# Kernel tuning notes

Measured on AMD Instinct MI355X. Metric: run time of the kernel, lower is better.

The kernel has to match this reference:

```python
import jax, jax.numpy as jnp
import numpy as np

C = 16          # cardinality (hard-coded in GraphHead)
E = 1024        # node_encoding_size == representation_size (residual requires equality)
S = 1024        # spatial_head output size (hard-coded Linear(256,1024))
R = 1024        # representation_size
D = R // C      # sub_repr_size = 64
NS, NO = 64, 256
NUM_ITER = 2
EPS = 1e-5


def _w(key, shape, fan_in):
    return jax.random.normal(key, shape, dtype=jnp.float32) * np.float32((2.0 / fan_in) ** 0.5)


def setup_inputs() -> dict:
    key = jax.random.key(0)
    ks = jax.random.split(key, 16)
    inp = {
        'h': jax.random.normal(ks[0], (NS, E), dtype=jnp.float32),
        'o': jax.random.normal(ks[1], (NO, E), dtype=jnp.float32),
        'spatial': jax.random.normal(ks[2], (NS, NO, S), dtype=jnp.float32),
        # attention_head: MultiBranchFusion(2E, 1024, R, 16)
        'att_w1': _w(ks[3], (C, 2 * E, D), 2 * E), 'att_b1': jnp.zeros((C, D), jnp.float32),
        'att_w2': _w(ks[4], (C, S, D), S),         'att_b2': jnp.zeros((C, D), jnp.float32),
        'att_w3': _w(ks[5], (C, D, R), D),         'att_b3': jnp.zeros((C, R), jnp.float32),
        # sub_to_obj: MessageMBF(E, 1024, R, 'subject', 16)
        's2o_w1': _w(ks[6], (C, E, D), E),         's2o_b1': jnp.zeros((C, D), jnp.float32),
        's2o_w2': _w(ks[7], (C, S, D), S),         's2o_b2': jnp.zeros((C, D), jnp.float32),
        's2o_w3': _w(ks[8], (C, D, R), D),         's2o_b3': jnp.zeros((C, R), jnp.float32),
        # obj_to_sub: MessageMBF(E, 1024, R, 'object', 16)
        'o2s_w1': _w(ks[9], (C, E, D), E),         'o2s_b1': jnp.zeros((C, D), jnp.float32),
        'o2s_w2': _w(ks[10], (C, S, D), S),        'o2s_b2': jnp.zeros((C, D), jnp.float32),
        'o2s_w3': _w(ks[11], (C, D, R), D),        'o2s_b3': jnp.zeros((C, R), jnp.float32),
        # adjacency: Linear(R, 1)
        'adj_w': _w(ks[12], (R, 1), R), 'adj_b': jnp.zeros((1,), jnp.float32),
        # LayerNorms
        'ns_g': jnp.ones((E,), jnp.float32), 'ns_b': jnp.zeros((E,), jnp.float32),
        'no_g': jnp.ones((E,), jnp.float32), 'no_b': jnp.zeros((E,), jnp.float32),
    }
    return inp


def _layernorm(x, g, b):
    m = jnp.mean(x, axis=-1, keepdims=True)
    v = jnp.mean((x - m) ** 2, axis=-1, keepdims=True)
    return (x - m) * jax.lax.rsqrt(v + EPS) * g + b


def _mbf_pair(app, spa, w1, b1, w2, b2, w3, b3):
    # app [ns,no,A], spa [ns,no,S] -> [ns,no,R]; sum over C branches of fc3(relu(fc1*fc2))
    a = jnp.einsum('ija,cad->cijd', app, w1) + b1[:, None, None, :]
    s = jnp.einsum('ijs,csd->cijd', spa, w2) + b2[:, None, None, :]
    g = jax.nn.relu(a * s)
    return jnp.einsum('cijd,cdr->ijr', g, w3) + b3.sum(0)


def _msg_subject(h, spa, w1, b1, w2, b2, w3, b3):
    # MessageMBF subject: broadcast fc1(h) [ns,d] against fc2(spa) [ns,no,d]
    a = jnp.einsum('ia,cad->cid', h, w1) + b1[:, None, :]
    s = jnp.einsum('ijs,csd->cijd', spa, w2) + b2[:, None, None, :]
    g = jax.nn.relu(a[:, :, None, :] * s)
    return jnp.einsum('cijd,cdr->ijr', g, w3) + b3.sum(0)  # [ns,no,R]


def _msg_object(o, spa, w1, b1, w2, b2, w3, b3):
    # MessageMBF object: broadcast fc1(o) [no,d] against fc2(spa) [ns,no,d]
    a = jnp.einsum('ja,cad->cjd', o, w1) + b1[:, None, :]
    s = jnp.einsum('ijs,csd->cijd', spa, w2) + b2[:, None, None, :]
    g = jax.nn.relu(a[:, None, :, :] * s)
    return jnp.einsum('cijd,cdr->ijr', g, w3) + b3.sum(0)  # [ns,no,R]


def reference(h, o, spatial,
              att_w1, att_b1, att_w2, att_b2, att_w3, att_b3,
              s2o_w1, s2o_b1, s2o_w2, s2o_b2, s2o_w3, s2o_b3,
              o2s_w1, o2s_b1, o2s_w2, o2s_b2, o2s_w3, o2s_b3,
              adj_w, adj_b, ns_g, ns_b, no_g, no_b):
    ns, no = h.shape[0], o.shape[0]
    for _ in range(NUM_ITER):
        # edge weights via attention MBF on concatenated pair encodings
        pair_app = jnp.concatenate([
            jnp.broadcast_to(h[:, None, :], (ns, no, E)),
            jnp.broadcast_to(o[None, :, :], (ns, no, E)),
        ], axis=-1)
        w = jax.nn.relu(_mbf_pair(pair_app, spatial, att_w1, att_b1, att_w2, att_b2, att_w3, att_b3))
        adj = jnp.einsum('ijr,rk->ij', w, adj_w) + adj_b[0]  # [ns,no]
        # update subject nodes from object messages
        m_o2s = _msg_object(o, spatial, o2s_w1, o2s_b1, o2s_w2, o2s_b2, o2s_w3, o2s_b3)
        msg_h = jax.nn.relu(jnp.einsum('ij,ijr->ir', jax.nn.softmax(adj, axis=1), m_o2s))
        h = _layernorm(h + msg_h, ns_g, ns_b)
        # update object nodes from (updated) subject messages
        m_s2o = _msg_subject(h, spatial, s2o_w1, s2o_b1, s2o_w2, s2o_b2, s2o_w3, s2o_b3)
        msg_o = jax.nn.relu(jnp.einsum('ij,ijr->jr', jax.nn.softmax(adj, axis=0), m_s2o))
        o = _layernorm(o + msg_o, no_g, no_b)
    return jnp.concatenate([h, o], axis=0)  # [ns+no, E]
```

## Files before the change

### kernel.cpp

```cpp
#include <hip/hip_runtime.h>
#include <cstdint>
#include <cstddef>

typedef _Float16 hf;
typedef _Float16 h8v __attribute__((ext_vector_type(8)));
typedef float f4v __attribute__((ext_vector_type(4)));

#define NS 64
#define NO 256
#define MP 16384
#define KD 1024

__device__ __forceinline__ h8v cvt8(float4 a, float4 b) {
    h8v r;
    r[0] = (hf)a.x; r[1] = (hf)a.y; r[2] = (hf)a.z; r[3] = (hf)a.w;
    r[4] = (hf)b.x; r[5] = (hf)b.y; r[6] = (hf)b.z; r[7] = (hf)b.w;
    return r;
}
__device__ __forceinline__ float f4at(const float4& a, const float4& b, int e) {
    const float* p = e < 4 ? (const float*)&a : (const float*)&b;
    return p[e & 3];
}
__device__ __forceinline__ void gl16(const hf* g, hf* l) {
    __builtin_amdgcn_global_load_lds(
        (const __attribute__((address_space(1))) void*)g,
        (__attribute__((address_space(3))) void*)l, 16, 0, 0);
}

__global__ void k_pack16(const float* __restrict__ src, hf* __restrict__ dst, int n8) {
    int g = blockIdx.x * 256 + threadIdx.x;
    if (g >= n8) return;
    const float4* s4 = (const float4*)src;
    float4 a = s4[2 * g], b = s4[2 * g + 1];
    *(h8v*)(dst + (size_t)g * 8) = cvt8(a, b);
}

struct RoR { const float* src; hf* dhi; hf* dlo; int Asrc; int aOff; };
struct RoRs { RoR r[7]; };
__global__ void k_reorder16b(RoRs RR) {
    const RoR rt = RR.r[blockIdx.z];
    __shared__ float tile[64][65];
    int c = blockIdx.x, a0 = blockIdx.y * 64;
    int t = threadIdx.x, lx = t & 63, ly = t >> 6;
#pragma unroll
    for (int p = 0; p < 16; ++p) {
        int ar = ly + p * 4;
        tile[ar][lx] = rt.src[(size_t)(c * rt.Asrc + rt.aOff + a0 + ar) * 64 + lx];
    }
    __syncthreads();
#pragma unroll
    for (int p = 0; p < 16; ++p) {
        int d = ly + p * 4;
        float v = tile[lx][d];
        hf h = (hf)v;
        size_t idx = (size_t)(c * 64 + d) * 1024 + a0 + lx;
        rt.dhi[idx] = h;
        if (rt.dlo) rt.dlo[idx] = (hf)(v - (float)h);
    }
}

struct TrR { const float* src; hf* dhi; hf* dlo; };
struct TrRs { TrR r[3]; };
__global__ void k_transpose16b(TrRs RR) {
    const TrR rt = RR.r[blockIdx.z];
    __shared__ float tile[64][65];
    int r0 = blockIdx.x * 64, s0 = blockIdx.y * 64;
    int t = threadIdx.x, lx = t & 63, ly = t >> 6;
#pragma unroll
    for (int p = 0; p < 16; ++p) {
        int srow = ly + p * 4;
        tile[srow][lx] = rt.src[(size_t)(s0 + srow) * 1024 + r0 + lx];
    }
    __syncthreads();
#pragma unroll
    for (int p = 0; p < 16; ++p) {
        int rr = ly + p * 4;
        float v = tile[lx][rr];
        hf h = (hf)v;
        size_t idx = (size_t)(r0 + rr) * 1024 + s0 + lx;
        rt.dhi[idx] = h;
        if (rt.dlo) rt.dlo[idx] = (hf)(v - (float)h);
    }
}

__global__ void k_prep_bc(const float* __restrict__ ab2, const float* __restrict__ ob2,
                          const float* __restrict__ sb2, const float* __restrict__ ab3,
                          const float* __restrict__ ob3, const float* __restrict__ sb3,
                          float* __restrict__ b2cat, float* __restrict__ b3a,
                          float* __restrict__ b3o, float* __restrict__ b3s) {
    int g = blockIdx.x * 256 + threadIdx.x;
    if (g >= 1024) return;
    b2cat[g] = ab2[g]; b2cat[1024 + g] = ob2[g]; b2cat[2048 + g] = sb2[g];
    float sa = 0.f, so = 0.f, ss = 0.f;
    for (int c = 0; c < 16; ++c) {
        sa += ab3[c * 1024 + g];
        so += ob3[c * 1024 + g];
        ss += sb3[c * 1024 + g];
    }
    b3a[g] = sa; b3o[g] = so; b3s[g] = ss;
}

__global__ void k_init_ho(const float* __restrict__ h, const float* __restrict__ o,
                          float* __restrict__ outbuf, hf* __restrict__ h16, hf* __restrict__ o16) {
    int g = blockIdx.x * 256 + threadIdx.x;
    if (g < NS * KD) { float v = h[g]; outbuf[g] = v; h16[g] = (hf)v; }
    int g2 = g - NS * KD;
    if (g2 >= 0 && g2 < NO * KD) { float v = o[g2]; outbuf[NS * KD + g2] = v; o16[g2] = (hf)v; }
}

__global__ __launch_bounds__(256, 4) void k_prep_gemm(
    const hf* __restrict__ sp16,
    const hf* __restrict__ Wah, const hf* __restrict__ Wal,
    const hf* __restrict__ Wo2, const hf* __restrict__ Ws2,
    const float* __restrict__ b2cat,
    hf* __restrict__ Sh, hf* __restrict__ Sl,
    hf* __restrict__ So, hf* __restrict__ Ss) {
    __shared__ hf Ah[4096];
    __shared__ hf Bh[4096];
    __shared__ hf Bl[4096];
    const int tid = threadIdx.x;
    int lin = blockIdx.y * 24 + blockIdx.x;
    int xcd = lin & 7, slot = lin >> 3;
    int xn = slot % 24;
    const int m0 = ((xcd << 4) + slot / 24) * 128;
    const int plane = xn >> 3;
    const int nbase = (xn & 7) * 128;
    const hf* Bb = plane == 0 ? Wah : (plane == 1 ? Wo2 : Ws2);
    const bool hasL = (plane == 0);
    const int lane = tid & 63, wid = tid >> 6;
    const int wm = wid >> 1, wn = wid & 1;
    const int lr = lane & 15, lg = lane >> 4;
    const int rsl = (lg ^ ((lr >> 1) & 3)) * 8;

    const int crow = lane >> 2;
    const int gseg = ((lane & 3) ^ ((lane >> 3) & 3)) * 8;
    hf* ldsA0 = Ah + wid * 512;         hf* ldsA1 = Ah + 2048 + wid * 512;
    hf* ldsB0 = Bh + wid * 512;         hf* ldsB1 = Bh + 2048 + wid * 512;
    hf* ldsL0 = Bl + wid * 512;         hf* ldsL1 = Bl + 2048 + wid * 512;
    const hf* gA0 = sp16 + (size_t)(m0 +      wid * 16 + crow) * KD + gseg;
    const hf* gA1 = sp16 + (size_t)(m0 + 64 + wid * 16 + crow) * KD + gseg;
    const hf* gB0 = Bb  + (size_t)(nbase +      wid * 16 + crow) * KD + gseg;
    const hf* gB1 = Bb  + (size_t)(nbase + 64 + wid * 16 + crow) * KD + gseg;
    const hf* gL0 = Wal + (size_t)(nbase +      wid * 16 + crow) * KD + gseg;
    const hf* gL1 = Wal + (size_t)(nbase + 64 + wid * 16 + crow) * KD + gseg;

    f4v acc[4][4];
    f4v zz; zz[0] = 0.f; zz[1] = 0.f; zz[2] = 0.f; zz[3] = 0.f;
#pragma unroll
    for (int a = 0; a < 4; ++a)
#pragma unroll
        for (int b = 0; b < 4; ++b) acc[a][b] = zz;

    for (int t = 0; t < 32; ++t) {
        const int kk = t * 32;
        __syncthreads();
        gl16(gA0 + kk, ldsA0); gl16(gA1 + kk, ldsA1);
        gl16(gB0 + kk, ldsB0); gl16(gB1 + kk, ldsB1);
        if (hasL) { gl16(gL0 + kk, ldsL0); gl16(gL1 + kk, ldsL1); }
        __syncthreads();
        h8v fa[4], fb[4];
#pragma unroll
        for (int x = 0; x < 4; ++x) {
            fa[x] = *(const h8v*)(Ah + (wm * 64 + x * 16 + lr) * 32 + rsl);
            fb[x] = *(const h8v*)(Bh + (wn * 64 + x * 16 + lr) * 32 + rsl);
        }
#pragma unroll
        for (int mi = 0; mi < 4; ++mi)
#pragma unroll
            for (int ni = 0; ni < 4; ++ni)
                acc[mi][ni] = __builtin_amdgcn_mfma_f32_16x16x32_f16(fa[mi], fb[ni], acc[mi][ni], 0, 0, 0);
        if (hasL) {
#pragma unroll
            for (int x = 0; x < 4; ++x)
                fb[x] = *(const h8v*)(Bl + (wn * 64 + x * 16 + lr) * 32 + rsl);
#pragma unroll
            for (int mi = 0; mi < 4; ++mi)
#pragma unroll
                for (int ni = 0; ni < 4; ++ni)
                    acc[mi][ni] = __builtin_amdgcn_mfma_f32_16x16x32_f16(fa[mi], fb[ni], acc[mi][ni], 0, 0, 0);
        }
    }
#pragma unroll
    for (int mi = 0; mi < 4; ++mi)
#pragma unroll
        for (int ni = 0; ni < 4; ++ni)
#pragma unroll
            for (int r = 0; r < 4; ++r) {
                int gr = m0 + wm * 64 + mi * 16 + lg * 4 + r;
                int col = nbase + wn * 64 + ni * 16 + lr;
                float v = acc[mi][ni][r] + b2cat[plane * 1024 + col];
                size_t idx = (size_t)gr * KD + col;
                if (plane == 0) {
                    hf hi = (hf)v;
                    Sh[idx] = hi; Sl[idx] = (hf)(v - (float)hi);
                } else if (plane == 1) So[idx] = (hf)v;
                else Ss[idx] = (hf)v;
            }
}

__global__ __launch_bounds__(256, 3) void k_adj_gemm(
    const hf* __restrict__ Sh, const hf* __restrict__ Sl,
    const float* __restrict__ e1, const float* __restrict__ e2,
    const hf* __restrict__ W3h, const hf* __restrict__ W3l,
    const float* __restrict__ b3, const float* __restrict__ aw,
    float* __restrict__ adjv) {
    __shared__ hf Ah[4096];
    __shared__ hf Bh[4096];
    __shared__ hf Bl[4096];
    const int tid = threadIdx.x;
    int lin = blockIdx.y * 8 + blockIdx.x;
    int xcd = lin & 7, slot = lin >> 3;
    const int nbase = (slot & 7) * 128;
    const int m0 = ((xcd << 4) + (slot >> 3)) * 128;
    const int lane = tid & 63, wid = tid >> 6;
    const int wm = wid >> 1, wn = wid & 1;
    const int lr = lane & 15, lg = lane >> 4;
    const int srow = tid >> 2, sseg = tid & 3;
    const int wo_ = srow * 32 + (sseg ^ ((srow >> 1) & 3)) * 8;
    const int rsl = (lg ^ ((lr >> 1) & 3)) * 8;
    const int ar0 = m0 + srow, ar1 = ar0 + 64;
    const int i0 = ar0 >> 8, j0 = ar0 & 255;
    const int i1 = ar1 >> 8, j1 = ar1 & 255;
    const int ko = sseg * 8;

    f4v acc[4][4];
    f4v zz; zz[0] = 0.f; zz[1] = 0.f; zz[2] = 0.f; zz[3] = 0.f;
#pragma unroll
    for (int a = 0; a < 4; ++a)
#pragma unroll
        for (int b = 0; b < 4; ++b) acc[a][b] = zz;

    h8v sh0, sl0, sh1, sl1;
    float4 ex00, ex01, ey00, ey01, ex10, ex11, ey10, ey11;
    h8v vb0, vb1, wb0, wb1;
    h8v gh0, gh1;
    auto LOAD = [&](int kk) {
        sh0 = *(const h8v*)(Sh + (size_t)ar0 * KD + ko + kk);
        sl0 = *(const h8v*)(Sl + (size_t)ar0 * KD + ko + kk);
        sh1 = *(const h8v*)(Sh + (size_t)ar1 * KD + ko + kk);
        sl1 = *(const h8v*)(Sl + (size_t)ar1 * KD + ko + kk);
        ex00 = *(const float4*)(e1 + (size_t)i0 * KD + ko + kk);
        ex01 = *(const float4*)(e1 + (size_t)i0 * KD + ko + kk + 4);
        ey00 = *(const float4*)(e2 + (size_t)j0 * KD + ko + kk);
        ey01 = *(const float4*)(e2 + (size_t)j0 * KD + ko + kk + 4);
        ex10 = *(const float4*)(e1 + (size_t)i1 * KD + ko + kk);
        ex11 = *(const float4*)(e1 + (size_t)i1 * KD + ko + kk + 4);
        ey10 = *(const float4*)(e2 + (size_t)j1 * KD + ko + kk);
        ey11 = *(const float4*)(e2 + (size_t)j1 * KD + ko + kk + 4);
        vb0 = *(const h8v*)(W3h + (size_t)(nbase + srow) * KD + ko + kk);
        vb1 = *(const h8v*)(W3h + (size_t)(nbase + 64 + srow) * KD + ko + kk);
        wb0 = *(const h8v*)(W3l + (size_t)(nbase + srow) * KD + ko + kk);
        wb1 = *(const h8v*)(W3l + (size_t)(nbase + 64 + srow) * KD + ko + kk);
    };
    auto BUILD = [&]() {
#pragma unroll
        for (int e = 0; e < 8; ++e) {
            float s = (float)sh0[e] + (float)sl0[e];
            float ee = f4at(ex00, ex01, e) + f4at(ey00, ey01, e);
            float gg = ee * s; gg = gg > 0.f ? gg : 0.f;
            gh0[e] = (hf)gg;
        }
#pragma unroll
        for (int e = 0; e < 8; ++e) {
            float s = (float)sh1[e] + (float)sl1[e];
            float ee = f4at(ex10, ex11, e) + f4at(ey10, ey11, e);
            float gg = ee * s; gg = gg > 0.f ? gg : 0.f;
            gh1[e] = (hf)gg;
        }
    };
    LOAD(0);
    BUILD();
    for (int t = 0; t < 32; ++t) {
        __syncthreads();
        *(h8v*)(Ah + wo_) = gh0; *(h8v*)(Ah + 2048 + wo_) = gh1;
        *(h8v*)(Bh + wo_) = vb0; *(h8v*)(Bh + 2048 + wo_) = vb1;
        *(h8v*)(Bl + wo_) = wb0; *(h8v*)(Bl + 2048 + wo_) = wb1;
        __syncthreads();
        if (t + 1 < 32) { LOAD((t + 1) * 32); BUILD(); }
        h8v fa[4], fb[4];
#pragma unroll
        for (int x = 0; x < 4; ++x) {
            fa[x] = *(const h8v*)(Ah + (wm * 64 + x * 16 + lr) * 32 + rsl);
            fb[x] = *(const h8v*)(Bh + (wn * 64 + x * 16 + lr) * 32 + rsl);
        }
#pragma unroll
        for (int mi = 0; mi < 4; ++mi)
#pragma unroll
            for (int ni = 0; ni < 4; ++ni)
                acc[mi][ni] = __builtin_amdgcn_mfma_f32_16x16x32_f16(fa[mi], fb[ni], acc[mi][ni], 0, 0, 0);
#pragma unroll
        for (int x = 0; x < 4; ++x)
            fb[x] = *(const h8v*)(Bl + (wn * 64 + x * 16 + lr) * 32 + rsl);
#pragma unroll
        for (int mi = 0; mi < 4; ++mi)
#pragma unroll
            for (int ni = 0; ni < 4; ++ni)
                acc[mi][ni] = __builtin_amdgcn_mfma_f32_16x16x32_f16(fa[mi], fb[ni], acc[mi][ni], 0, 0, 0);
    }
    float b3v[4], awv[4];
#pragma unroll
    for (int ni = 0; ni < 4; ++ni) {
        int gc = nbase + wn * 64 + ni * 16 + lr;
        b3v[ni] = b3[gc]; awv[ni] = aw[gc];
    }
#pragma unroll
    for (int mi = 0; mi < 4; ++mi)
#pragma unroll
        for (int r = 0; r < 4; ++r) {
            float part = 0.f;
#pragma unroll
            for (int ni = 0; ni < 4; ++ni) {
                float w = acc[mi][ni][r] + b3v[ni];
                w = w > 0.f ? w : 0.f;
                part += w * awv[ni];
            }
            part += __shfl_xor(part, 1);
            part += __shfl_xor(part, 2);
            part += __shfl_xor(part, 4);
            part += __shfl_xor(part, 8);
            if (lr == 0) atomicAdd(adjv + m0 + wm * 64 + mi * 16 + lg * 4 + r, part);
        }
}

struct SRoute { const hf* A; const hf* Bh; const hf* Bl; float* C; const float* bias; int m0; int M; };
struct SRoutes { SRoute r[5]; };

__global__ __launch_bounds__(256) void k_small(SRoutes RR) {
    const SRoute rt = RR.r[blockIdx.y];
    __shared__ hf Ah[4096];
    __shared__ hf Bh[4096];
    __shared__ hf Bl[4096];
    const int tid = threadIdx.x;
    const int n0 = blockIdx.x * 128;
    const int kbeg = blockIdx.z * 128;
    const int lane = tid & 63, wid = tid >> 6;
    const int wm = wid >> 1, wn = wid & 1;
    const int lr = lane & 15, lg = lane >> 4;
    const int srow = tid >> 2, sseg = tid & 3;
    const int wo_ = srow * 32 + (sseg ^ ((srow >> 1) & 3)) * 8;
    const int rsl = (lg ^ ((lr >> 1) & 3)) * 8;
    int ar0 = rt.m0 + srow;      if (ar0 >= rt.M) ar0 = rt.M - 1;
    int ar1 = rt.m0 + 64 + srow; if (ar1 >= rt.M) ar1 = rt.M - 1;
    const bool hasL = rt.Bl != nullptr;
    const int ko = kbeg + sseg * 8;

    f4v acc[4][4];
    f4v zz; zz[0] = 0.f; zz[1] = 0.f; zz[2] = 0.f; zz[3] = 0.f;
#pragma unroll
    for (int a = 0; a < 4; ++a)
#pragma unroll
        for (int b = 0; b < 4; ++b) acc[a][b] = zz;

    h8v va0, va1, vb0, vb1, wb0, wb1;
    auto LOAD = [&](int kk) {
        va0 = *(const h8v*)(rt.A + (size_t)ar0 * KD + ko + kk);
        va1 = *(const h8v*)(rt.A + (size_t)ar1 * KD + ko + kk);
        vb0 = *(const h8v*)(rt.Bh + (size_t)(n0 + srow) * KD + ko + kk);
        vb1 = *(const h8v*)(rt.Bh + (size_t)(n0 + 64 + srow) * KD + ko + kk);
        if (hasL) {
            wb0 = *(const h8v*)(rt.Bl + (size_t)(n0 + srow) * KD + ko + kk);
            wb1 = *(const h8v*)(rt.Bl + (size_t)(n0 + 64 + srow) * KD + ko + kk);
        }
    };
    LOAD(0);
    for (int t = 0; t < 4; ++t) {
        __syncthreads();
        *(h8v*)(Ah + wo_) = va0; *(h8v*)(Ah + 2048 + wo_) = va1;
        *(h8v*)(Bh + wo_) = vb0; *(h8v*)(Bh + 2048 + wo_) = vb1;
        if (hasL) { *(h8v*)(Bl + wo_) = wb0; *(h8v*)(Bl + 2048 + wo_) = wb1; }
        __syncthreads();
        if (t + 1 < 4) LOAD((t + 1) * 32);
        h8v fa[4], fb[4];
#pragma unroll
        for (int x = 0; x < 4; ++x) {
            fa[x] = *(const h8v*)(Ah + (wm * 64 + x * 16 + lr) * 32 + rsl);
            fb[x] = *(const h8v*)(Bh + (wn * 64 + x * 16 + lr) * 32 + rsl);
        }
#pragma unroll
        for (int mi = 0; mi < 4; ++mi)
#pragma unroll
            for (int ni = 0; ni < 4; ++ni)
                acc[mi][ni] = __builtin_amdgcn_mfma_f32_16x16x32_f16(fa[mi], fb[ni], acc[mi][ni], 0, 0, 0);
        if (hasL) {
#pragma unroll
            for (int x = 0; x < 4; ++x)
                fb[x] = *(const h8v*)(Bl + (wn * 64 + x * 16 + lr) * 32 + rsl);
#pragma unroll
            for (int mi = 0; mi < 4; ++mi)
#pragma unroll
                for (int ni = 0; ni < 4; ++ni)
                    acc[mi][ni] = __builtin_amdgcn_mfma_f32_16x16x32_f16(fa[mi], fb[ni], acc[mi][ni], 0, 0, 0);
        }
    }
#pragma unroll
    for (int mi = 0; mi < 4; ++mi)
#pragma unroll
        for (int ni = 0; ni < 4; ++ni)
#pragma unroll
            for (int r = 0; r < 4; ++r) {
                int gr = rt.m0 + wm * 64 + mi * 16 + lg * 4 + r;
                int gc = n0 + wn * 64 + ni * 16 + lr;
                if (gr < rt.M) {
                    float v = acc[mi][ni][r];
                    if (rt.bias && blockIdx.z == 0) v += rt.bias[gc];
                    atomicAdd(rt.C + (size_t)gr * KD + gc, v);
                }
            }
}

__global__ void k_softmax_both(const float* __restrict__ adj, float* __restrict__ p,
                               float* __restrict__ q) {
    int b = blockIdx.x;
    if (b < NS) {
        __shared__ float red[256];
        int i = b, j = threadIdx.x;
        float x = adj[i * 256 + j];
        red[j] = x; __syncthreads();
        for (int s = 128; s > 0; s >>= 1) { if (j < s) red[j] = fmaxf(red[j], red[j + s]); __syncthreads(); }
        float mx = red[0]; __syncthreads();
        float e = __expf(x - mx);
        red[j] = e; __syncthreads();
        for (int s = 128; s > 0; s >>= 1) { if (j < s) red[j] += red[j + s]; __syncthreads(); }
        p[i * 256 + j] = e / red[0];
    } else {
        int j = (b - NS) * 4 + (threadIdx.x >> 6);
        int i = threadIdx.x & 63;
        float x = adj[i * 256 + j];
        float mx = x;
#pragma unroll
        for (int off = 32; off > 0; off >>= 1) mx = fmaxf(mx, __shfl_xor(mx, off));
        float e = __expf(x - mx);
        float s = e;
#pragma unroll
        for (int off = 32; off > 0; off >>= 1) s += __shfl_xor(s, off);
        q[i * 256 + j] = e / s;
    }
}

__global__ void k_build_Gh(const hf* __restrict__ S, const float* __restrict__ aF,
                           const float* __restrict__ p, hf* __restrict__ Gh) {
    __shared__ float pl[256];
    int i = blockIdx.x;
    int k = blockIdx.y * 256 + threadIdx.x;
    pl[threadIdx.x] = p[i * 256 + threadIdx.x];
    __syncthreads();
    const hf* sp = S + (size_t)(i * 256) * KD + k;
    float acc = 0.f;
#pragma unroll 4
    for (int j = 0; j < 256; ++j) {
        float a = aF[(size_t)j * KD + k];
        float s = (float)sp[(size_t)j * KD];
        float g = a * s; g = g > 0.f ? g : 0.f;
        acc += pl[j] * g;
    }
    Gh[(size_t)i * KD + k] = (hf)acc;
}

__global__ void k_build_Go(const hf* __restrict__ S, const float* __restrict__ aF,
                           const float* __restrict__ q, hf* __restrict__ Go) {
    __shared__ float ql[64];
    int j = blockIdx.x;
    int k = blockIdx.y * 256 + threadIdx.x;
    if (threadIdx.x < 64) ql[threadIdx.x] = q[threadIdx.x * 256 + j];
    __syncthreads();
    const hf* sp = S + (size_t)j * KD + k;
    float acc = 0.f;
#pragma unroll 4
    for (int i = 0; i < 64; ++i) {
        float a = aF[(size_t)i * KD + k];
        float s = (float)sp[(size_t)(i * 256) * KD];
        float g = a * s; g = g > 0.f ? g : 0.f;
        acc += ql[i] * g;
    }
    Go[(size_t)j * KD + k] = (hf)acc;
}

__global__ void k_ln_update(float* __restrict__ x, const float* __restrict__ msg,
                            const float* __restrict__ b3, const float* __restrict__ gamma,
                            const float* __restrict__ beta, hf* __restrict__ x16) {
    __shared__ float red[256];
    int r = blockIdx.x, t = threadIdx.x;
    float v[4];
    float s = 0.f;
#pragma unroll
    for (int e = 0; e < 4; ++e) {
        int idx = t + e * 256;
        float mm = msg[(size_t)r * KD + idx] + b3[idx];
        mm = mm > 0.f ? mm : 0.f;
        v[e] = x[(size_t)r * KD + idx] + mm;
        s += v[e];
    }
    red[t] = s; __syncthreads();
    for (int st = 128; st > 0; st >>= 1) { if (t < st) red[t] += red[t + st]; __syncthreads(); }
    float mean = red[0] * (1.f / 1024.f);
    __syncthreads();
    float s2 = 0.f;
#pragma unroll
    for (int e = 0; e < 4; ++e) { float d = v[e] - mean; s2 += d * d; }
    red[t] = s2; __syncthreads();
    for (int st = 128; st > 0; st >>= 1) { if (t < st) red[t] += red[t + st]; __syncthreads(); }
    float var = red[0] * (1.f / 1024.f);
    float rstd = rsqrtf(var + 1e-5f);
#pragma unroll
    for (int e = 0; e < 4; ++e) {
        int idx = t + e * 256;
        float y = (v[e] - mean) * rstd * gamma[idx] + beta[idx];
        x[(size_t)r * KD + idx] = y;
        x16[(size_t)r * KD + idx] = (hf)y;
    }
}

extern "C" void kernel_launch(void* const* d_in, const int* in_sizes, int n_in,
                              void* d_out, int out_size, void* d_ws, size_t ws_size,
                              hipStream_t stream) {
    const float* h_in    = (const float*)d_in[0];
    const float* o_in    = (const float*)d_in[1];
    const float* spatial = (const float*)d_in[2];
    const float* att_w1  = (const float*)d_in[3];
    const float* att_b1  = (const float*)d_in[4];
    const float* att_w2  = (const float*)d_in[5];
    const float* att_b2  = (const float*)d_in[6];
    const float* att_w3  = (const float*)d_in[7];
    const float* att_b3  = (const float*)d_in[8];
    const float* s2o_w1  = (const float*)d_in[9];
    const float* s2o_b1  = (const float*)d_in[10];
    const float* s2o_w2  = (const float*)d_in[11];
    const float* s2o_b2  = (const float*)d_in[12];
    const float* s2o_w3  = (const float*)d_in[13];
    const float* s2o_b3  = (const float*)d_in[14];
    const float* o2s_w1  = (const float*)d_in[15];
    const float* o2s_b1  = (const float*)d_in[16];
    const float* o2s_w2  = (const float*)d_in[17];
    const float* o2s_b2  = (const float*)d_in[18];
    const float* o2s_w3  = (const float*)d_in[19];
    const float* o2s_b3  = (const float*)d_in[20];
    const float* adj_w   = (const float*)d_in[21];
    const float* ns_g    = (const float*)d_in[23];
    const float* ns_b    = (const float*)d_in[24];
    const float* no_g    = (const float*)d_in[25];
    const float* no_b    = (const float*)d_in[26];

    char* ws = (char*)d_ws;
    size_t off = 0;
    auto alloc = [&](size_t bytes) -> char* {
        char* pp = ws + off;
        off += (bytes + 255) & ~(size_t)255;
        return pp;
    };
    const size_t PLANE = (size_t)MP * KD * sizeof(hf);
    const size_t WMAT  = (size_t)1024 * 1024 * sizeof(hf);
    hf* S_att_h = (hf*)alloc(PLANE);
    hf* S_att_l = (hf*)alloc(PLANE);
    hf* S_o2s   = (hf*)alloc(PLANE);
    hf* S_s2o   = (hf*)alloc(PLANE);
    hf* sp16    = (hf*)alloc(PLANE);
    hf* W2att_h = (hf*)alloc(WMAT); hf* W2att_l = (hf*)alloc(WMAT);
    hf* W2o2s   = (hf*)alloc(WMAT);
    hf* W2s2o   = (hf*)alloc(WMAT);
    hf* W1ah_h  = (hf*)alloc(WMAT); hf* W1ah_l  = (hf*)alloc(WMAT);
    hf* W1ao_h  = (hf*)alloc(WMAT); hf* W1ao_l  = (hf*)alloc(WMAT);
    hf* W1o2s   = (hf*)alloc(WMAT);
    hf* W1s2o   = (hf*)alloc(WMAT);
    hf* W3a_h   = (hf*)alloc(WMAT); hf* W3a_l   = (hf*)alloc(WMAT);
    hf* W3o     = (hf*)alloc(WMAT);
    hf* W3s     = (hf*)alloc(WMAT);
    float* b2cat = (float*)alloc(3072 * 4);
    float* b3a   = (float*)alloc(1024 * 4);
    float* b3o   = (float*)alloc(1024 * 4);
    float* b3s   = (float*)alloc(1024 * 4);
    float* fc1h = (float*)alloc((size_t)NS * KD * 4);
    float* fc1o = (float*)alloc((size_t)NO * KD * 4);
    float* aO2S = (float*)alloc((size_t)NO * KD * 4);
    float* aS2O = (float*)alloc((size_t)NS * KD * 4);
    float* msgh = (float*)alloc((size_t)NS * KD * 4);
    float* msgo = (float*)alloc((size_t)NO * KD * 4);
    float* adjv = (float*)alloc((size_t)MP * 4);
    char* zend_ = (char*)(adjv + MP);
    size_t zlen = (size_t)(zend_ - (char*)fc1h);
    float* pbuf = (float*)alloc((size_t)MP * 4);
    float* qbuf = (float*)alloc((size_t)MP * 4);
    hf* h16 = (hf*)alloc((size_t)NS * KD * sizeof(hf));
    hf* o16 = (hf*)alloc((size_t)NO * KD * sizeof(hf));
    hf* Gh  = (hf*)alloc((size_t)NS * KD * sizeof(hf));
    hf* Go  = (hf*)alloc((size_t)NO * KD * sizeof(hf));

    float* hbuf = (float*)d_out;
    float* obuf = (float*)d_out + NS * KD;

    k_pack16<<<dim3(MP * KD / 8 / 256), 256, 0, stream>>>(spatial, sp16, MP * KD / 8);
    {
        RoRs R;
        R.r[0] = { att_w2, W2att_h, W2att_l, 1024, 0 };
        R.r[1] = { o2s_w2, W2o2s, nullptr, 1024, 0 };
        R.r[2] = { s2o_w2, W2s2o, nullptr, 1024, 0 };
        R.r[3] = { att_w1, W1ah_h, W1ah_l, 2048, 0 };
        R.r[4] = { att_w1, W1ao_h, W1ao_l, 2048, 1024 };
        R.r[5] = { o2s_w1, W1o2s, nullptr, 1024, 0 };
        R.r[6] = { s2o_w1, W1s2o, nullptr, 1024, 0 };
        k_reorder16b<<<dim3(16, 16, 7), 256, 0, stream>>>(R);
    }
    {
        TrRs T;
        T.r[0] = { att_w3, W3a_h, W3a_l };
        T.r[1] = { o2s_w3, W3o, nullptr };
        T.r[2] = { s2o_w3, W3s, nullptr };
        k_transpose16b<<<dim3(16, 16, 3), 256, 0, stream>>>(T);
    }
    k_prep_bc<<<dim3(4), 256, 0, stream>>>(att_b2, o2s_b2, s2o_b2, att_b3, o2s_b3, s2o_b3,
                                           b2cat, b3a, b3o, b3s);
    k_init_ho<<<dim3(1280), 256, 0, stream>>>(h_in, o_in, (float*)d_out, h16, o16);
    k_prep_gemm<<<dim3(24, 128), 256, 0, stream>>>(sp16, W2att_h, W2att_l, W2o2s, W2s2o,
                                                   b2cat, S_att_h, S_att_l, S_o2s, S_s2o);

    for (int it = 0; it < 2; ++it) {
        hipMemsetAsync(fc1h, 0, zlen, stream);
        {
            SRoutes R;
            R.r[0] = { h16, W1ah_h, W1ah_l, fc1h, att_b1, 0,   NS };
            R.r[1] = { o16, W1ao_h, W1ao_l, fc1o, nullptr, 0,   NO };
            R.r[2] = { o16, W1ao_h, W1ao_l, fc1o, nullptr, 128, NO };
            R.r[3] = { o16, W1o2s,  nullptr, aO2S, o2s_b1, 0,   NO };
            R.r[4] = { o16, W1o2s,  nullptr, aO2S, o2s_b1, 128, NO };
            k_small<<<dim3(8, 5, 8), 256, 0, stream>>>(R);
        }
        k_adj_gemm<<<dim3(8, 128), 256, 0, stream>>>(S_att_h, S_att_l, fc1h, fc1o,
                                                     W3a_h, W3a_l, b3a, adj_w, adjv);
        k_softmax_both<<<dim3(NS + NO / 4), 256, 0, stream>>>(adjv, pbuf, qbuf);
        k_build_Gh<<<dim3(NS, 4), 256, 0, stream>>>(S_o2s, aO2S, pbuf, Gh);
        {
            SRoutes R;
            R.r[0] = { Gh, W3o, nullptr, msgh, nullptr, 0, NS };
            k_small<<<dim3(8, 1, 8), 256, 0, stream>>>(R);
        }
        k_ln_update<<<dim3(NS), 256, 0, stream>>>(hbuf, msgh, b3o, ns_g, ns_b, h16);
        {
            SRoutes R;
            R.r[0] = { h16, W1s2o, nullptr, aS2O, s2o_b1, 0, NS };
            k_small<<<dim3(8, 1, 8), 256, 0, stream>>>(R);
        }
        k_build_Go<<<dim3(NO, 4), 256, 0, stream>>>(S_s2o, aS2O, qbuf, Go);
        {
            SRoutes R;
            R.r[0] = { Go, W3s, nullptr, msgo, nullptr, 0,   NO };
            R.r[1] = { Go, W3s, nullptr, msgo, nullptr, 128, NO };
            k_small<<<dim3(8, 2, 8), 256, 0, stream>>>(R);
        }
        k_ln_update<<<dim3(NO), 256, 0, stream>>>(obuf, msgo, b3s, no_g, no_b, o16);
    }
    (void)in_sizes; (void)n_in; (void)out_size; (void)ws_size;
}
```

Measured before the change: 739.1 us.

## Widen adjacency GEMM N-tile to 256 to amortize A-operand construction

The fused adjacency GEMM now has each block cover 256 output columns instead of 128, using two accumulator sets and doubled B tiles in LDS, and the grid is halved accordingly. The A operand (relu of pair encoding times spatial) is loaded and built elementwise per block, so this halves the redundant global loads and construction of A across N-tiles. In exchange it doubles accumulator registers and raises LDS use, with launch bounds lowered from 3 to 2 blocks per CU, which reduces occupancy and the total number of blocks.

```diff
diff --git a/kernel.cpp b/kernel.cpp
--- a/kernel.cpp
+++ b/kernel.cpp
@@ -198,20 +198,20 @@
             }
 }
 
-__global__ __launch_bounds__(256, 3) void k_adj_gemm(
+__global__ __launch_bounds__(256, 2) void k_adj_gemm(
     const hf* __restrict__ Sh, const hf* __restrict__ Sl,
     const float* __restrict__ e1, const float* __restrict__ e2,
     const hf* __restrict__ W3h, const hf* __restrict__ W3l,
     const float* __restrict__ b3, const float* __restrict__ aw,
     float* __restrict__ adjv) {
     __shared__ hf Ah[4096];
-    __shared__ hf Bh[4096];
-    __shared__ hf Bl[4096];
+    __shared__ hf Bh[8192];
+    __shared__ hf Bl[8192];
     const int tid = threadIdx.x;
-    int lin = blockIdx.y * 8 + blockIdx.x;
+    int lin = blockIdx.y * 4 + blockIdx.x;
     int xcd = lin & 7, slot = lin >> 3;
-    const int nbase = (slot & 7) * 128;
-    const int m0 = ((xcd << 4) + (slot >> 3)) * 128;
+    const int nbase = (slot & 3) * 256;
+    const int m0 = ((xcd << 4) + (slot >> 2)) * 128;
     const int lane = tid & 63, wid = tid >> 6;
     const int wm = wid >> 1, wn = wid & 1;
     const int lr = lane & 15, lg = lane >> 4;
@@ -223,16 +223,18 @@
     const int i1 = ar1 >> 8, j1 = ar1 & 255;
     const int ko = sseg * 8;
 
-    f4v acc[4][4];
+    f4v acc[2][4][4];
     f4v zz; zz[0] = 0.f; zz[1] = 0.f; zz[2] = 0.f; zz[3] = 0.f;
 #pragma unroll
-    for (int a = 0; a < 4; ++a)
-#pragma unroll
-        for (int b = 0; b < 4; ++b) acc[a][b] = zz;
+    for (int u = 0; u < 2; ++u)
+#pragma unroll
+        for (int a = 0; a < 4; ++a)
+#pragma unroll
+            for (int b = 0; b < 4; ++b) acc[u][a][b] = zz;
 
     h8v sh0, sl0, sh1, sl1;
     float4 ex00, ex01, ey00, ey01, ex10, ex11, ey10, ey11;
-    h8v vb0, vb1, wb0, wb1;
+    h8v vb00, vb01, vb10, vb11, wb00, wb01, wb10, wb11;
     h8v gh0, gh1;
     auto LOAD = [&](int kk) {
         sh0 = *(const h8v*)(Sh + (size_t)ar0 * KD + ko + kk);
@@ -247,10 +249,14 @@
         ex11 = *(const float4*)(e1 + (size_t)i1 * KD + ko + kk + 4);
         ey10 = *(const float4*)(e2 + (size_t)j1 * KD + ko + kk);
         ey11 = *(const float4*)(e2 + (size_t)j1 * KD + ko + kk + 4);
-        vb0 = *(const h8v*)(W3h + (size_t)(nbase + srow) * KD + ko + kk);
-        vb1 = *(const h8v*)(W3h + (size_t)(nbase + 64 + srow) * KD + ko + kk);
-        wb0 = *(const h8v*)(W3l + (size_t)(nbase + srow) * KD + ko + kk);
-        wb1 = *(const h8v*)(W3l + (size_t)(nbase + 64 + srow) * KD + ko + kk);
+        vb00 = *(const h8v*)(W3h + (size_t)(nbase + srow) * KD + ko + kk);
+        vb01 = *(const h8v*)(W3h + (size_t)(nbase + 64 + srow) * KD + ko + kk);
+        vb10 = *(const h8v*)(W3h + (size_t)(nbase + 128 + srow) * KD + ko + kk);
+        vb11 = *(const h8v*)(W3h + (size_t)(nbase + 192 + srow) * KD + ko + kk);
+        wb00 = *(const h8v*)(W3l + (size_t)(nbase + srow) * KD + ko + kk);
+        wb01 = *(const h8v*)(W3l + (size_t)(nbase + 64 + srow) * KD + ko + kk);
+        wb10 = *(const h8v*)(W3l + (size_t)(nbase + 128 + srow) * KD + ko + kk);
+        wb11 = *(const h8v*)(W3l + (size_t)(nbase + 192 + srow) * KD + ko + kk);
     };
     auto BUILD = [&]() {
 #pragma unroll
@@ -273,47 +279,57 @@
     for (int t = 0; t < 32; ++t) {
         __syncthreads();
         *(h8v*)(Ah + wo_) = gh0; *(h8v*)(Ah + 2048 + wo_) = gh1;
-        *(h8v*)(Bh + wo_) = vb0; *(h8v*)(Bh + 2048 + wo_) = vb1;
-        *(h8v*)(Bl + wo_) = wb0; *(h8v*)(Bl + 2048 + wo_) = wb1;
+        *(h8v*)(Bh + wo_) = vb00; *(h8v*)(Bh + 2048 + wo_) = vb01;
+        *(h8v*)(Bh + 4096 + wo_) = vb10; *(h8v*)(Bh + 6144 + wo_) = vb11;
+        *(h8v*)(Bl + wo_) = wb00; *(h8v*)(Bl + 2048 + wo_) = wb01;
+        *(h8v*)(Bl + 4096 + wo_) = wb10; *(h8v*)(Bl + 6144 + wo_) = wb11;
         __syncthreads();
         if (t + 1 < 32) { LOAD((t + 1) * 32); BUILD(); }
         h8v fa[4], fb[4];
 #pragma unroll
-        for (int x = 0; x < 4; ++x) {
+        for (int x = 0; x < 4; ++x)
             fa[x] = *(const h8v*)(Ah + (wm * 64 + x * 16 + lr) * 32 + rsl);
-            fb[x] = *(const h8v*)(Bh + (wn * 64 + x * 16 + lr) * 32 + rsl);
-        }
-#pragma unroll
-        for (int mi = 0; mi < 4; ++mi)
-#pragma unroll
-            for (int ni = 0; ni < 4; ++ni)
-                acc[mi][ni] = __builtin_amdgcn_mfma_f32_16x16x32_f16(fa[mi], fb[ni], acc[mi][ni], 0, 0, 0);
-#pragma unroll
-        for (int x = 0; x < 4; ++x)
-            fb[x] = *(const h8v*)(Bl + (wn * 64 + x * 16 + lr) * 32 + rsl);
-#pragma unroll
-        for (int mi = 0; mi < 4; ++mi)
-#pragma unroll
-            for (int ni = 0; ni < 4; ++ni)
-                acc[mi][ni] = __builtin_amdgcn_mfma_f32_16x16x32_f16(fa[mi], fb[ni], acc[mi][ni], 0, 0, 0);
-    }
-    float b3v[4], awv[4];
-#pragma unroll
-    for (int ni = 0; ni < 4; ++ni) {
-        int gc = nbase + wn * 64 + ni * 16 + lr;
-        b3v[ni] = b3[gc]; awv[ni] = aw[gc];
-    }
+#pragma unroll
+        for (int u = 0; u < 2; ++u) {
+#pragma unroll
+            for (int x = 0; x < 4; ++x)
+                fb[x] = *(const h8v*)(Bh + u * 4096 + (wn * 64 + x * 16 + lr) * 32 + rsl);
+#pragma unroll
+            for (int mi = 0; mi < 4; ++mi)
+#pragma unroll
+                for (int ni = 0; ni < 4; ++ni)
+                    acc[u][mi][ni] = __builtin_amdgcn_mfma_f32_16x16x32_f16(fa[mi], fb[ni], acc[u][mi][ni], 0, 0, 0);
+#pragma unroll
+            for (int x = 0; x < 4; ++x)
+                fb[x] = *(const h8v*)(Bl + u * 4096 + (wn * 64 + x * 16 + lr) * 32 + rsl);
+#pragma unroll
+            for (int mi = 0; mi < 4; ++mi)
+#pragma unroll
+                for (int ni = 0; ni < 4; ++ni)
+                    acc[u][mi][ni] = __builtin_amdgcn_mfma_f32_16x16x32_f16(fa[mi], fb[ni], acc[u][mi][ni], 0, 0, 0);
+        }
+    }
+    float b3v[2][4], awv[2][4];
+#pragma unroll
+    for (int u = 0; u < 2; ++u)
+#pragma unroll
+        for (int ni = 0; ni < 4; ++ni) {
+            int gc = nbase + u * 128 + wn * 64 + ni * 16 + lr;
+            b3v[u][ni] = b3[gc]; awv[u][ni] = aw[gc];
+        }
 #pragma unroll
     for (int mi = 0; mi < 4; ++mi)
 #pragma unroll
         for (int r = 0; r < 4; ++r) {
             float part = 0.f;
 #pragma unroll
-            for (int ni = 0; ni < 4; ++ni) {
-                float w = acc[mi][ni][r] + b3v[ni];
-                w = w > 0.f ? w : 0.f;
-                part += w * awv[ni];
-            }
+            for (int u = 0; u < 2; ++u)
+#pragma unroll
+                for (int ni = 0; ni < 4; ++ni) {
+                    float w = acc[u][mi][ni][r] + b3v[u][ni];
+                    w = w > 0.f ? w : 0.f;
+                    part += w * awv[u][ni];
+                }
             part += __shfl_xor(part, 1);
             part += __shfl_xor(part, 2);
             part += __shfl_xor(part, 4);
@@ -623,7 +639,7 @@
             R.r[4] = { o16, W1o2s,  nullptr, aO2S, o2s_b1, 128, NO };
             k_small<<<dim3(8, 5, 8), 256, 0, stream>>>(R);
         }
-        k_adj_gemm<<<dim3(8, 128), 256, 0, stream>>>(S_att_h, S_att_l, fc1h, fc1o,
+        k_adj_gemm<<<dim3(4, 128), 256, 0, stream>>>(S_att_h, S_att_l, fc1h, fc1o,
                                                      W3a_h, W3a_l, b3a, adj_w, adjv);
         k_softmax_both<<<dim3(NS + NO / 4), 256, 0, stream>>>(adjv, pbuf, qbuf);
         k_build_Gh<<<dim3(NS, 4), 256, 0, stream>>>(S_o2s, aO2S, pbuf, Gh);
```

New measurement: 614.7 us. -16.8%, faster.
